# Performance work log

Measured on AMD Instinct MI355X. Metric: run time of the kernel, lower is better.

The kernel has to match this reference:

```python
import jax, jax.numpy as jnp
import numpy as np

B, SQ, SK = 8, 128, 128
IVD, DIM, EV, H, NH = 32, 32, 64, 8, 128
DK = EV // H


def setup_inputs() -> dict:
    key = jax.random.key(0)
    ks = jax.random.split(key, 16)
    n = lambda k, s: jax.random.normal(k, s, dtype=jnp.float32)
    lin = lambda k, fi, fo: n(k, (fi, fo)) / np.float32(np.sqrt(fi))
    d = {}
    d['query_value'] = n(ks[0], (B, SQ, IVD))
    d['key_value']   = n(ks[1], (B, SK, IVD))
    d['value']       = n(ks[2], (B, SK, DIM))
    d['impute_data'] = n(ks[3], (B, SQ, IVD // 2))
    d['emb_mask'] = jax.random.randint(ks[4], (B, SK, DIM), 0, 2).astype(jnp.int32)
    # learn_value_embedding: Linear(IVD,NH)+Tanh+Linear(NH,EV,no bias)
    d['w1'] = lin(ks[5], IVD, NH); d['b1'] = jnp.zeros((NH,), jnp.float32)
    d['w2'] = lin(ks[6], NH, EV)
    # linears[0], linears[1]: Linear(EV,EV)
    d['wq'] = lin(ks[7], EV, EV); d['bq'] = jnp.zeros((EV,), jnp.float32)
    d['wk'] = lin(ks[8], EV, EV); d['bk'] = jnp.zeros((EV,), jnp.float32)
    # linears[2]: Linear(DIM*H, NH)
    d['wo'] = lin(ks[9], DIM * H, NH); d['bo'] = jnp.zeros((NH,), jnp.float32)
    # query_data_enc: Linear(IVD/2,NH)+LayerNorm(NH)+ReLU+Linear(NH,NH)
    d['wd1'] = lin(ks[10], IVD // 2, NH); d['bd1'] = jnp.zeros((NH,), jnp.float32)
    d['ln_g'] = jnp.ones((NH,), jnp.float32); d['ln_b'] = jnp.zeros((NH,), jnp.float32)
    d['wd2'] = lin(ks[11], NH, NH); d['bd2'] = jnp.zeros((NH,), jnp.float32)
    return d


def reference(query_value, key_value, value, impute_data,
              w1, b1, w2, wq, bq, wk, bk, wo, bo,
              wd1, bd1, ln_g, ln_b, wd2, bd2, emb_mask):
    b = query_value.shape[0]
    dim = value.shape[-1]
    # value embeddings: Linear -> Tanh -> Linear(no bias)
    qe = jnp.tanh(query_value @ w1 + b1) @ w2   # [B,Sq,EV]
    ke = jnp.tanh(key_value @ w1 + b1) @ w2     # [B,Sk,EV]
    q = (qe @ wq + bq).reshape(b, -1, H, DK).transpose(0, 2, 1, 3)  # [B,H,Sq,DK]
    k = (ke @ wk + bk).reshape(b, -1, H, DK).transpose(0, 2, 1, 3)  # [B,H,Sk,DK]
    scores = jnp.einsum('bhqd,bhkd->bhqk', q, k) / np.float32(np.sqrt(DK))
    # broadcast scores over the value channel dim; masked_fill with -10000
    m = emb_mask[:, None, None, :, :]           # [B,1,1,Sk,dim]
    logits = jnp.where(m == 0, jnp.float32(-10000.0), scores[..., None])  # [B,H,Sq,Sk,dim]
    p_attn = jax.nn.softmax(logits, axis=-2)    # softmax over Sk per channel
    out = jnp.einsum('bhqkd,bkd->bhqd', p_attn, value)  # [B,H,Sq,dim]
    x = out.transpose(0, 2, 1, 3).reshape(b, -1, H * dim)
    y = x @ wo + bo                             # [B,Sq,NH]
    # query_data_enc branch
    h1 = impute_data @ wd1 + bd1
    mu = jnp.mean(h1, axis=-1, keepdims=True)
    var = jnp.var(h1, axis=-1, keepdims=True)
    ln = (h1 - mu) / jnp.sqrt(var + 1e-5) * ln_g + ln_b
    query_data = jax.nn.relu(ln) @ wd2 + bd2    # [B,Sq,NH]
    return y, query_data
```

## Files before the change

### kernel.cpp

```cpp
#include <hip/hip_runtime.h>
#include <math.h>

#define B 8
#define SQ 128
#define SK 128
#define IVD 32
#define DIM 32
#define EV 64
#define H 8
#define NH 128
#define DK 8
#define TQ 2
#define KG 8
#define PAD 132

__device__ __forceinline__ float fast_tanh(float x) {
    const float xc = fminf(fmaxf(x, -10.f), 10.f);
    const float t = __expf(2.f * xc);
    return (t - 1.f) / (t + 1.f);
}

__global__ __launch_bounds__(256, 2) void fused_all(
    const float* __restrict__ qv, const float* __restrict__ kv,
    const float* __restrict__ value, const int* __restrict__ mask,
    const float* __restrict__ imp,
    const float* __restrict__ w1, const float* __restrict__ b1,
    const float* __restrict__ w2,
    const float* __restrict__ wq, const float* __restrict__ bqv,
    const float* __restrict__ wk, const float* __restrict__ bkv,
    const float* __restrict__ wo, const float* __restrict__ bo,
    const float* __restrict__ wd1, const float* __restrict__ bd1,
    const float* __restrict__ ln_g, const float* __restrict__ ln_b,
    const float* __restrict__ wd2, const float* __restrict__ bd2,
    float* __restrict__ y, float* __restrict__ qd,
    float* __restrict__ kproj, unsigned long long* __restrict__ flags)
{
    const int blk = blockIdx.x;
    const int b = blk >> 6;
    const int q0 = (blk & 63) * TQ;
    const int r0 = blk * 2;
    const int tid = threadIdx.x;
    const int half = tid >> 7;
    const int t = tid & 127;

    const unsigned long long MAGIC = 0x85EBCA6B9E3779B9ull;

    __shared__ __align__(16) float qs[TQ * EV];
    __shared__ __align__(16) float sc[TQ * H * SK];
    __shared__ __align__(16) float mvt[DIM * PAD];
    __shared__ __align__(16) float mmt[DIM * PAD];
    __shared__ __align__(16) float2 part[H * KG * DIM];
    __shared__ __align__(16) float xr[TQ * H * DIM];
    __shared__ __align__(16) float ypart[2 * TQ * NH];
    __shared__ float xs[2][2][IVD];
    __shared__ float h1[2][2][NH];
    __shared__ float ev[2][2][EV];
    __shared__ float pA[2][2][128];
    __shared__ float xs2[2][IVD / 2];
    __shared__ float h1b[2][NH];
    __shared__ float redm[2][2];
    __shared__ float redv[2][2];

    for (int idx = tid; idx < SK * DIM; idx += 256) {
        const int k = idx >> 5, d = idx & 31;
        const float v = value[b * SK * DIM + idx];
        const float m = (float)mask[b * SK * DIM + idx];
        mvt[d * PAD + k] = v * m;
        mmt[d * PAD + k] = m;
    }

    {
        const float* src = half ? kv : qv;
        const float* wp  = half ? wk : wq;
        const float* bp  = half ? bkv : bqv;

        if (t < 2 * IVD) xs[half][t >> 5][t & 31] = src[r0 * IVD + t];
        __syncthreads();

        float a0 = b1[t], a1 = a0;
        #pragma unroll
        for (int i = 0; i < IVD; ++i) {
            const float w = w1[i * NH + t];
            a0 += xs[half][0][i] * w; a1 += xs[half][1][i] * w;
        }
        h1[half][0][t] = fast_tanh(a0);
        h1[half][1][t] = fast_tanh(a1);
        __syncthreads();

        const int o = t & 63, hf = t >> 6;
        {
            float c0 = 0.f, c1 = 0.f;
            #pragma unroll 8
            for (int i = hf * 64; i < hf * 64 + 64; ++i) {
                const float w = w2[i * EV + o];
                c0 += h1[half][0][i] * w; c1 += h1[half][1][i] * w;
            }
            pA[half][0][t] = c0; pA[half][1][t] = c1;
        }
        __syncthreads();
        {
            const int row = t >> 6, oo = t & 63;
            ev[half][row][oo] = pA[half][row][oo] + pA[half][row][oo + 64];
        }
        __syncthreads();
        {
            float c0 = 0.f, c1 = 0.f;
            #pragma unroll 8
            for (int j = hf * 32; j < hf * 32 + 32; ++j) {
                const float w = wp[j * EV + o];
                c0 += ev[half][0][j] * w; c1 += ev[half][1][j] * w;
            }
            pA[half][0][t] = c0; pA[half][1][t] = c1;
        }
        __syncthreads();
        {
            const int row = t >> 6, oo = t & 63;
            const float res = pA[half][row][oo] + pA[half][row][oo + 64] + bp[oo];
            if (half == 0) qs[row * EV + oo] = res * 0.3535533905932738f;
            else           kproj[(r0 + row) * EV + oo] = res;
        }
    }
    __syncthreads();
    if (tid == 0) {
        __builtin_amdgcn_fence(__ATOMIC_RELEASE, "agent");
        __hip_atomic_store(&flags[blk], MAGIC, __ATOMIC_RELAXED,
                           __HIP_MEMORY_SCOPE_AGENT);
    }

    {
        if (tid < IVD) xs2[tid >> 4][tid & 15] = imp[r0 * (IVD / 2) + tid];
        __syncthreads();
        float a = bd1[t];
        #pragma unroll
        for (int i = 0; i < IVD / 2; ++i)
            a += xs2[half][i] * wd1[i * NH + t];

        float s = a;
        #pragma unroll
        for (int off = 32; off > 0; off >>= 1) s += __shfl_down(s, off, 64);
        if ((t & 63) == 0) redm[half][t >> 6] = s;
        __syncthreads();
        const float mu = (redm[half][0] + redm[half][1]) * (1.f / NH);
        const float d = a - mu;
        float v2 = d * d;
        #pragma unroll
        for (int off = 32; off > 0; off >>= 1) v2 += __shfl_down(v2, off, 64);
        if ((t & 63) == 0) redv[half][t >> 6] = v2;
        __syncthreads();
        const float var = (redv[half][0] + redv[half][1]) * (1.f / NH);

        h1b[half][t] = fmaxf(d * rsqrtf(var + 1e-5f) * ln_g[t] + ln_b[t], 0.f);
        __syncthreads();

        float c = bd2[t];
        #pragma unroll 8
        for (int j = 0; j < NH; ++j)
            c += h1b[half][j] * wd2[j * NH + t];
        qd[(r0 + half) * NH + t] = c;
    }

    {
        const unsigned long long* fb = flags + b * 64;
        const int lane = tid & 63;
        for (int it = 0; it < (1 << 22); ++it) {
            const unsigned long long v = __hip_atomic_load(
                &fb[lane], __ATOMIC_RELAXED, __HIP_MEMORY_SCOPE_AGENT);
            if (__all(v == MAGIC)) break;
            __builtin_amdgcn_s_sleep(2);
        }
        __builtin_amdgcn_fence(__ATOMIC_ACQUIRE, "agent");
    }
    __syncthreads();

    #pragma unroll
    for (int i = 0; i < (TQ * H * SK) / 256; ++i) {
        const int p = tid + i * 256;
        const int q = p >> 10, rem = p & 1023, h = rem >> 7, k = rem & 127;
        const float4* kr = (const float4*)(kproj + (b * SK + k) * EV + h * DK);
        const float4* qq = (const float4*)(qs + q * EV + h * DK);
        const float4 k0 = kr[0], k1 = kr[1], qa = qq[0], qb = qq[1];
        const float s = qa.x * k0.x + qa.y * k0.y + qa.z * k0.z + qa.w * k0.w
                      + qb.x * k1.x + qb.y * k1.y + qb.z * k1.z + qb.w * k1.w;
        sc[p] = __expf(s);
    }
    __syncthreads();

    {
        const int d = tid & 31, kg = tid >> 5;
        float4 vv[4], mq[4];
        const float4* vp = (const float4*)&mvt[d * PAD + kg * 16];
        const float4* mp = (const float4*)&mmt[d * PAD + kg * 16];
        #pragma unroll
        for (int j = 0; j < 4; ++j) { vv[j] = vp[j]; mq[j] = mp[j]; }

        #pragma unroll
        for (int q = 0; q < TQ; ++q) {
            #pragma unroll
            for (int h = 0; h < H; ++h) {
                const float4* sp = (const float4*)&sc[(q * H + h) * SK + kg * 16];
                float num = 0.f, den = 0.f;
                #pragma unroll
                for (int j = 0; j < 4; ++j) {
                    const float4 s = sp[j];
                    num += s.x * vv[j].x + s.y * vv[j].y + s.z * vv[j].z + s.w * vv[j].w;
                    den += s.x * mq[j].x + s.y * mq[j].y + s.z * mq[j].z + s.w * mq[j].w;
                }
                part[(h * KG + kg) * DIM + d] = make_float2(num, den);
            }
            __syncthreads();
            {
                const int h = tid >> 5;
                float num = 0.f, den = 0.f;
                #pragma unroll
                for (int g = 0; g < KG; ++g) {
                    const float2 p2 = part[(h * KG + g) * DIM + d];
                    num += p2.x; den += p2.y;
                }
                xr[q * (H * DIM) + tid] = num / den;
            }
            __syncthreads();
        }
    }

    {
        const int n = tid & 127, hh = tid >> 7;
        const float* wop = wo + hh * 128 * NH + n;
        const float* x0 = xr + hh * 128;
        const float* x1 = xr + (H * DIM) + hh * 128;
        float a0 = 0.f, a1 = 0.f;
        #pragma unroll 4
        for (int j = 0; j < 128; ++j) {
            const float w = wop[j * NH];
            a0 += w * x0[j];
            a1 += w * x1[j];
        }
        ypart[hh * (TQ * NH) + 0 * NH + n] = a0;
        ypart[hh * (TQ * NH) + 1 * NH + n] = a1;
    }
    __syncthreads();
    {
        const int q = tid >> 7, n = tid & 127;
        y[(b * SQ + q0 + q) * NH + n] =
            ypart[q * NH + n] + ypart[TQ * NH + q * NH + n] + bo[n];
    }
}

extern "C" void kernel_launch(void* const* d_in, const int* in_sizes, int n_in,
                              void* d_out, int out_size, void* d_ws, size_t ws_size,
                              hipStream_t stream) {
    const float* query_value = (const float*)d_in[0];
    const float* key_value   = (const float*)d_in[1];
    const float* value       = (const float*)d_in[2];
    const float* impute      = (const float*)d_in[3];
    const int*   emb_mask    = (const int*)d_in[4];
    const float* w1   = (const float*)d_in[5];
    const float* b1   = (const float*)d_in[6];
    const float* w2   = (const float*)d_in[7];
    const float* wq   = (const float*)d_in[8];
    const float* bq   = (const float*)d_in[9];
    const float* wk   = (const float*)d_in[10];
    const float* bk   = (const float*)d_in[11];
    const float* wo   = (const float*)d_in[12];
    const float* bo   = (const float*)d_in[13];
    const float* wd1  = (const float*)d_in[14];
    const float* bd1  = (const float*)d_in[15];
    const float* ln_g = (const float*)d_in[16];
    const float* ln_b = (const float*)d_in[17];
    const float* wd2  = (const float*)d_in[18];
    const float* bd2  = (const float*)d_in[19];

    float* y  = (float*)d_out;
    float* qd = y + B * SQ * NH;

    float* kproj = (float*)d_ws;
    unsigned long long* flags =
        (unsigned long long*)((char*)d_ws + B * SK * EV * sizeof(float));

    hipLaunchKernelGGL(fused_all, dim3(512), dim3(256), 0, stream,
                       query_value, key_value, value, emb_mask, impute,
                       w1, b1, w2, wq, bq, wk, bk, wo, bo,
                       wd1, bd1, ln_g, ln_b, wd2, bd2,
                       y, qd, kproj, flags);
}
```

Before: 135.1 us.

## Load masked values into registers directly and share K loads across both queries

Drops the transposed shared-memory staging of value and mask (mvt/mmt). Each thread now loads its own strided column slice of value and mask from global memory straight into registers, which frees about 34KB of LDS per block. The score loop now loads each K row once and computes both query rows from it, using relaxed atomic loads in place of an acquire fence. The spin-wait sleep is also shortened. The global loads are strided and uncoalesced, and dropping the fence leans on per-load atomicity for memory ordering.

```diff
diff --git a/kernel.cpp b/kernel.cpp
--- a/kernel.cpp
+++ b/kernel.cpp
@@ -12,7 +12,6 @@
 #define DK 8
 #define TQ 2
 #define KG 8
-#define PAD 132
 
 __device__ __forceinline__ float fast_tanh(float x) {
     const float xc = fminf(fmaxf(x, -10.f), 10.f);
@@ -20,7 +19,7 @@
     return (t - 1.f) / (t + 1.f);
 }
 
-__global__ __launch_bounds__(256, 2) void fused_all(
+__global__ __launch_bounds__(256, 2) void fused_all2(
     const float* __restrict__ qv, const float* __restrict__ kv,
     const float* __restrict__ value, const int* __restrict__ mask,
     const float* __restrict__ imp,
@@ -37,7 +36,6 @@
 {
     const int blk = blockIdx.x;
     const int b = blk >> 6;
-    const int q0 = (blk & 63) * TQ;
     const int r0 = blk * 2;
     const int tid = threadIdx.x;
     const int half = tid >> 7;
@@ -47,8 +45,6 @@
 
     __shared__ __align__(16) float qs[TQ * EV];
     __shared__ __align__(16) float sc[TQ * H * SK];
-    __shared__ __align__(16) float mvt[DIM * PAD];
-    __shared__ __align__(16) float mmt[DIM * PAD];
     __shared__ __align__(16) float2 part[H * KG * DIM];
     __shared__ __align__(16) float xr[TQ * H * DIM];
     __shared__ __align__(16) float ypart[2 * TQ * NH];
@@ -61,12 +57,24 @@
     __shared__ float redm[2][2];
     __shared__ float redv[2][2];
 
-    for (int idx = tid; idx < SK * DIM; idx += 256) {
-        const int k = idx >> 5, d = idx & 31;
-        const float v = value[b * SK * DIM + idx];
-        const float m = (float)mask[b * SK * DIM + idx];
-        mvt[d * PAD + k] = v * m;
-        mmt[d * PAD + k] = m;
+    const int d = tid & 31, kg = tid >> 5;
+    float4 vv[4], mq[4];
+    {
+        const float* vb = value + b * SK * DIM + d;
+        const int*   mb = mask  + b * SK * DIM + d;
+        #pragma unroll
+        for (int j = 0; j < 4; ++j) {
+            const int k0 = kg * 16 + j * 4;
+            const float m0 = (float)mb[(k0 + 0) * DIM];
+            const float m1 = (float)mb[(k0 + 1) * DIM];
+            const float m2 = (float)mb[(k0 + 2) * DIM];
+            const float m3 = (float)mb[(k0 + 3) * DIM];
+            mq[j] = make_float4(m0, m1, m2, m3);
+            vv[j] = make_float4(vb[(k0 + 0) * DIM] * m0,
+                                vb[(k0 + 1) * DIM] * m1,
+                                vb[(k0 + 2) * DIM] * m2,
+                                vb[(k0 + 3) * DIM] * m3);
+        }
     }
 
     {
@@ -141,15 +149,15 @@
         if ((t & 63) == 0) redm[half][t >> 6] = s;
         __syncthreads();
         const float mu = (redm[half][0] + redm[half][1]) * (1.f / NH);
-        const float d = a - mu;
-        float v2 = d * d;
+        const float dd = a - mu;
+        float v2 = dd * dd;
         #pragma unroll
         for (int off = 32; off > 0; off >>= 1) v2 += __shfl_down(v2, off, 64);
         if ((t & 63) == 0) redv[half][t >> 6] = v2;
         __syncthreads();
         const float var = (redv[half][0] + redv[half][1]) * (1.f / NH);
 
-        h1b[half][t] = fmaxf(d * rsqrtf(var + 1e-5f) * ln_g[t] + ln_b[t], 0.f);
+        h1b[half][t] = fmaxf(dd * rsqrtf(var + 1e-5f) * ln_g[t] + ln_b[t], 0.f);
         __syncthreads();
 
         float c = bd2[t];
@@ -166,60 +174,60 @@
             const unsigned long long v = __hip_atomic_load(
                 &fb[lane], __ATOMIC_RELAXED, __HIP_MEMORY_SCOPE_AGENT);
             if (__all(v == MAGIC)) break;
-            __builtin_amdgcn_s_sleep(2);
-        }
-        __builtin_amdgcn_fence(__ATOMIC_ACQUIRE, "agent");
+            __builtin_amdgcn_s_sleep(1);
+        }
+        asm volatile("" ::: "memory");
+    }
+
+    #pragma unroll
+    for (int i = 0; i < (H * SK) / 256; ++i) {
+        const int p = tid + i * 256;
+        const int h = p >> 7, k = p & 127;
+        float* kr = kproj + (b * SK + k) * EV + h * DK;
+        float kf[8];
+        #pragma unroll
+        for (int j = 0; j < 8; ++j)
+            kf[j] = __hip_atomic_load(kr + j, __ATOMIC_RELAXED,
+                                      __HIP_MEMORY_SCOPE_AGENT);
+        const float4* qq0 = (const float4*)(qs + 0 * EV + h * DK);
+        const float4* qq1 = (const float4*)(qs + 1 * EV + h * DK);
+        const float4 qa = qq0[0], qb = qq0[1];
+        const float4 qc = qq1[0], qe = qq1[1];
+        const float s0 = qa.x * kf[0] + qa.y * kf[1] + qa.z * kf[2] + qa.w * kf[3]
+                       + qb.x * kf[4] + qb.y * kf[5] + qb.z * kf[6] + qb.w * kf[7];
+        const float s1 = qc.x * kf[0] + qc.y * kf[1] + qc.z * kf[2] + qc.w * kf[3]
+                       + qe.x * kf[4] + qe.y * kf[5] + qe.z * kf[6] + qe.w * kf[7];
+        sc[0 * (H * SK) + p] = __expf(s0);
+        sc[1 * (H * SK) + p] = __expf(s1);
     }
     __syncthreads();
 
     #pragma unroll
-    for (int i = 0; i < (TQ * H * SK) / 256; ++i) {
-        const int p = tid + i * 256;
-        const int q = p >> 10, rem = p & 1023, h = rem >> 7, k = rem & 127;
-        const float4* kr = (const float4*)(kproj + (b * SK + k) * EV + h * DK);
-        const float4* qq = (const float4*)(qs + q * EV + h * DK);
-        const float4 k0 = kr[0], k1 = kr[1], qa = qq[0], qb = qq[1];
-        const float s = qa.x * k0.x + qa.y * k0.y + qa.z * k0.z + qa.w * k0.w
-                      + qb.x * k1.x + qb.y * k1.y + qb.z * k1.z + qb.w * k1.w;
-        sc[p] = __expf(s);
-    }
-    __syncthreads();
-
-    {
-        const int d = tid & 31, kg = tid >> 5;
-        float4 vv[4], mq[4];
-        const float4* vp = (const float4*)&mvt[d * PAD + kg * 16];
-        const float4* mp = (const float4*)&mmt[d * PAD + kg * 16];
-        #pragma unroll
-        for (int j = 0; j < 4; ++j) { vv[j] = vp[j]; mq[j] = mp[j]; }
-
-        #pragma unroll
-        for (int q = 0; q < TQ; ++q) {
+    for (int q = 0; q < TQ; ++q) {
+        #pragma unroll
+        for (int h = 0; h < H; ++h) {
+            const float4* sp = (const float4*)&sc[(q * H + h) * SK + kg * 16];
+            float num = 0.f, den = 0.f;
             #pragma unroll
-            for (int h = 0; h < H; ++h) {
-                const float4* sp = (const float4*)&sc[(q * H + h) * SK + kg * 16];
-                float num = 0.f, den = 0.f;
-                #pragma unroll
-                for (int j = 0; j < 4; ++j) {
-                    const float4 s = sp[j];
-                    num += s.x * vv[j].x + s.y * vv[j].y + s.z * vv[j].z + s.w * vv[j].w;
-                    den += s.x * mq[j].x + s.y * mq[j].y + s.z * mq[j].z + s.w * mq[j].w;
-                }
-                part[(h * KG + kg) * DIM + d] = make_float2(num, den);
-            }
-            __syncthreads();
-            {
-                const int h = tid >> 5;
-                float num = 0.f, den = 0.f;
-                #pragma unroll
-                for (int g = 0; g < KG; ++g) {
-                    const float2 p2 = part[(h * KG + g) * DIM + d];
-                    num += p2.x; den += p2.y;
-                }
-                xr[q * (H * DIM) + tid] = num / den;
-            }
-            __syncthreads();
-        }
+            for (int j = 0; j < 4; ++j) {
+                const float4 s = sp[j];
+                num += s.x * vv[j].x + s.y * vv[j].y + s.z * vv[j].z + s.w * vv[j].w;
+                den += s.x * mq[j].x + s.y * mq[j].y + s.z * mq[j].z + s.w * mq[j].w;
+            }
+            part[(h * KG + kg) * DIM + d] = make_float2(num, den);
+        }
+        __syncthreads();
+        {
+            const int h2 = tid >> 5;
+            float num = 0.f, den = 0.f;
+            #pragma unroll
+            for (int g = 0; g < KG; ++g) {
+                const float2 p2 = part[(h2 * KG + g) * DIM + d];
+                num += p2.x; den += p2.y;
+            }
+            xr[q * (H * DIM) + tid] = num / den;
+        }
+        __syncthreads();
     }
 
     {
@@ -240,7 +248,7 @@
     __syncthreads();
     {
         const int q = tid >> 7, n = tid & 127;
-        y[(b * SQ + q0 + q) * NH + n] =
+        y[(r0 + q) * NH + n] =
             ypart[q * NH + n] + ypart[TQ * NH + q * NH + n] + bo[n];
     }
 }
@@ -276,7 +284,7 @@
     unsigned long long* flags =
         (unsigned long long*)((char*)d_ws + B * SK * EV * sizeof(float));
 
-    hipLaunchKernelGGL(fused_all, dim3(512), dim3(256), 0, stream,
+    hipLaunchKernelGGL(fused_all2, dim3(512), dim3(256), 0, stream,
                        query_value, key_value, value, emb_mask, impute,
                        w1, b1, w2, wq, bq, wk, bk, wo, bo,
                        wd1, bd1, ln_g, ln_b, wd2, bd2,
```

Result: no change. 132.7 us (-1.8%).
